# Kernel tuning notes

Hardware: AMD Instinct MI355X
Metric: run time of the kernel (lower is better)

Reference implementation:

```python
import jax, jax.numpy as jnp
import numpy as np

NEG_SLOPE = 0.2  # GATConv attention leaky_relu slope (init arg)
POST_SLOPE = 0.2  # leaky_relu after LayerNorm in outer forward
N_LAYERS = 3


def _leaky(x, slope):
    return jnp.where(x >= 0, x, slope * x)


def _layer_norm(x, g, b):
    mu = jnp.mean(x, axis=-1, keepdims=True)
    var = jnp.var(x, axis=-1, keepdims=True)
    return (x - mu) * jax.lax.rsqrt(var + 1e-5) * g + b


def _gat_conv(h, W, al, ar, bias, src, dst, apply_act):
    # DGL GATConv (eval mode, dropout = identity)
    N = h.shape[0]
    H, D = al.shape
    feat = (h @ W).reshape(N, H, D)                      # [N,H,D]
    el = jnp.einsum('nhd,hd->nh', feat, al)              # [N,H]
    er = jnp.einsum('nhd,hd->nh', feat, ar)              # [N,H]
    e = _leaky(el[src] + er[dst], NEG_SLOPE)             # [E,H] edge logits
    # segment (per-destination) softmax, numerically stable
    m = jax.ops.segment_max(e, dst, num_segments=N)      # [N,H]
    ex = jnp.exp(e - m[dst])                             # [E,H]
    s = jax.ops.segment_sum(ex, dst, num_segments=N)     # [N,H]
    alpha = ex / s[dst]                                  # [E,H]
    msg = alpha[:, :, None] * feat[src]                  # [E,H,D]
    rst = jax.ops.segment_sum(msg, dst, num_segments=N)  # [N,H,D]
    rst = rst + bias.reshape(1, H, D)
    if apply_act:
        rst = jax.nn.elu(rst)
    return rst


def setup_inputs() -> dict:
    key = jax.random.key(0)
    ks = jax.random.split(key, 12)
    N, E, IN, D, H, C = 100000, 1600000, 256, 64, 4, 40
    HID = H * D  # 256
    sc = 0.05
    return {
        'x': jax.random.normal(ks[0], (N, IN), jnp.float32),
        'W_h': jax.random.normal(ks[1], (3, IN, HID), jnp.float32) * sc,
        'attn_l_h': jax.random.normal(ks[2], (3, H, D), jnp.float32) * sc,
        'attn_r_h': jax.random.normal(ks[3], (3, H, D), jnp.float32) * sc,
        'bias_h': jnp.zeros((3, HID), jnp.float32),
        'ln_g': jnp.ones((3, HID), jnp.float32),
        'ln_b': jnp.zeros((3, HID), jnp.float32),
        'W_o': jax.random.normal(ks[4], (HID, C), jnp.float32) * sc,
        'attn_l_o': jax.random.normal(ks[5], (1, C), jnp.float32) * sc,
        'attn_r_o': jax.random.normal(ks[6], (1, C), jnp.float32) * sc,
        'bias_o': jnp.zeros((C,), jnp.float32),
        'edge_src': jax.random.randint(ks[7], (E,), 0, N, jnp.int32),
        'edge_dst': jax.random.randint(ks[8], (E,), 0, N, jnp.int32),
    }


def reference(x, W_h, attn_l_h, attn_r_h, bias_h, ln_g, ln_b,
              W_o, attn_l_o, attn_r_o, bias_o, edge_src, edge_dst):
    h = x
    for l in range(N_LAYERS):
        hn = _gat_conv(h, W_h[l], attn_l_h[l], attn_r_h[l], bias_h[l],
                       edge_src, edge_dst, True)
        hn = hn.reshape(hn.shape[0], -1)          # flatten heads -> [N, H*D]
        hn = _layer_norm(hn, ln_g[l], ln_b[l])
        hn = _leaky(hn, POST_SLOPE)
        h = hn + h if h.shape == hn.shape else hn  # residual when shapes match
    logits = _gat_conv(h, W_o, attn_l_o, attn_r_o, bias_o,
                       edge_src, edge_dst, False).sum(axis=1)  # sum over heads
    return logits
```

## Files before the change

### kernel.cpp

```cpp
#include <hip/hip_runtime.h>
#include <math.h>


#define NEG_SLOPE 0.2f

typedef __attribute__((ext_vector_type(8))) short bf16x8;
typedef __attribute__((ext_vector_type(4))) float floatx4;

__device__ __forceinline__ float leaky(float x) { return x >= 0.f ? x : NEG_SLOPE * x; }

__device__ __forceinline__ unsigned short f2bf(float f) {
    unsigned u = __builtin_bit_cast(unsigned, f);
    u += 0x7fffu + ((u >> 16) & 1u);
    return (unsigned short)(u >> 16);
}
__device__ __forceinline__ float bf2f(unsigned short h) {
    unsigned u = ((unsigned)h) << 16;
    return __builtin_bit_cast(float, u);
}

__global__ void zero_i32(int* __restrict__ p, int n) {
    int i = blockIdx.x * blockDim.x + threadIdx.x;
    if (i < n) p[i] = 0;
}

__global__ __launch_bounds__(256) void bucket_count(const int* __restrict__ dst,
                                                    int* __restrict__ bcnt, int E, int nbkt) {
    __shared__ int h[1024];
    for (int i = threadIdx.x; i < nbkt; i += 256) h[i] = 0;
    __syncthreads();
    const int base = blockIdx.x * 8192;
#pragma unroll 4
    for (int i = 0; i < 32; ++i) {
        int e = base + threadIdx.x + i * 256;
        if (e < E) atomicAdd(&h[dst[e] >> 7], 1);
    }
    __syncthreads();
    for (int i = threadIdx.x; i < nbkt; i += 256) {
        int v = h[i];
        if (v) atomicAdd(&bcnt[i], v);
    }
}

__global__ __launch_bounds__(256) void bucket_scan(const int* __restrict__ bcnt,
                                                   int* __restrict__ bbase,
                                                   int* __restrict__ bcursor, int nbkt) {
    __shared__ int s[256];
    const int t = threadIdx.x;
    int c[4];
    int tsum = 0;
#pragma unroll
    for (int j = 0; j < 4; ++j) {
        int i = t * 4 + j;
        c[j] = (i < nbkt) ? bcnt[i] : 0;
        tsum += c[j];
    }
    s[t] = tsum;
    __syncthreads();
    for (int off = 1; off < 256; off <<= 1) {
        int v = (t >= off) ? s[t - off] : 0;
        __syncthreads();
        s[t] += v;
        __syncthreads();
    }
    int excl = s[t] - tsum;
#pragma unroll
    for (int j = 0; j < 4; ++j) {
        int i = t * 4 + j;
        if (i < nbkt) {
            bbase[i] = excl;
            bcursor[i] = excl;
        }
        excl += c[j];
    }
}

__global__ __launch_bounds__(256) void bucket_partition(const int* __restrict__ src,
                                                        const int* __restrict__ dst,
                                                        int* __restrict__ bcursor,
                                                        int2* __restrict__ pairs, int E, int nbkt) {
    __shared__ int h[1024];
    __shared__ int basech[1024];
    for (int i = threadIdx.x; i < nbkt; i += 256) h[i] = 0;
    __syncthreads();
    const int base = blockIdx.x * 8192;
#pragma unroll 4
    for (int i = 0; i < 32; ++i) {
        int e = base + threadIdx.x + i * 256;
        if (e < E) atomicAdd(&h[dst[e] >> 7], 1);
    }
    __syncthreads();
    for (int i = threadIdx.x; i < nbkt; i += 256) {
        int v = h[i];
        basech[i] = v ? atomicAdd(&bcursor[i], v) : 0;
    }
    __syncthreads();
    for (int i = threadIdx.x; i < nbkt; i += 256) h[i] = 0;
    __syncthreads();
#pragma unroll 4
    for (int i = 0; i < 32; ++i) {
        int e = base + threadIdx.x + i * 256;
        if (e < E) {
            int d = dst[e], b = d >> 7;
            int r = atomicAdd(&h[b], 1);
            pairs[basech[b] + r] = make_int2(src[e], d);
        }
    }
}

__global__ __launch_bounds__(256) void csr_bucket(const int2* __restrict__ pairs,
                                                  const int* __restrict__ bbase,
                                                  int* __restrict__ start, int* __restrict__ endp,
                                                  int* __restrict__ col, int N, int E, int nbkt) {
    const int b = blockIdx.x;
    const int node0 = b << 7;
    int nc = N - node0;
    if (nc <= 0) return;
    if (nc > 128) nc = 128;
    __shared__ int cnt[128];
    __shared__ int s[128];
    const int t = threadIdx.x;
    if (t < 128) cnt[t] = 0;
    __syncthreads();
    const int ebase = bbase[b];
    const int eend = (b + 1 < nbkt) ? bbase[b + 1] : E;
    for (int e = ebase + t; e < eend; e += 256) {
        atomicAdd(&cnt[pairs[e].y - node0], 1);
    }
    __syncthreads();
    if (t < 128) s[t] = cnt[t];
    __syncthreads();
    for (int off = 1; off < 128; off <<= 1) {
        int v = 0;
        if (t < 128 && t >= off) v = s[t - off];
        __syncthreads();
        if (t < 128) s[t] += v;
        __syncthreads();
    }
    if (t < nc) {
        start[node0 + t] = ebase + s[t] - cnt[t];
        endp[node0 + t] = ebase + s[t];
    }
    if (t < 128) cnt[t] = s[t] - cnt[t];
    __syncthreads();
    for (int e = ebase + t; e < eend; e += 256) {
        int2 pr = pairs[e];
        int r = atomicAdd(&cnt[pr.y - node0], 1);
        col[ebase + r] = pr.x;
    }
}

__global__ void convert_bf(const float* __restrict__ src, unsigned short* __restrict__ dst,
                           int n4) {
    int i = blockIdx.x * blockDim.x + threadIdx.x;
    if (i < n4) {
        float4 v = *(const float4*)(src + (size_t)i * 4);
        ushort4 s;
        s.x = f2bf(v.x); s.y = f2bf(v.y); s.z = f2bf(v.z); s.w = f2bf(v.w);
        *(ushort4*)(dst + (size_t)i * 4) = s;
    }
}

__global__ void transpose_w(const float* __restrict__ W, unsigned short* __restrict__ Wt) {
    int idx = blockIdx.x * 256 + threadIdx.x;
    int l = idx >> 16, r = idx & 65535;
    int k = r >> 8, n = r & 255;
    Wt[l * 65536 + n * 256 + k] = f2bf(W[l * 65536 + k * 256 + n]);
}

__global__ void transpose_wo(const float* __restrict__ W, unsigned short* __restrict__ Wt) {
    int idx = blockIdx.x * 256 + threadIdx.x;
    int n = idx >> 8, k = idx & 255;
    Wt[n * 256 + k] = (n < 40) ? f2bf(W[k * 40 + n]) : (unsigned short)0;
}

#define BPAD 264
#define ALD 40
__global__ __launch_bounds__(512, 2) void gemm_bf16_fused(
    const unsigned short* __restrict__ A, const unsigned short* __restrict__ Wt,
    const float* __restrict__ al, const float* __restrict__ ar,
    unsigned short* __restrict__ Cb, float* __restrict__ el, float* __restrict__ er, int M) {
    __shared__ unsigned short Bs[256 * BPAD];
    __shared__ unsigned short As[2][128 * ALD];
    const int tid = threadIdx.x;
    const int lane = tid & 63, wid = tid >> 6;
    const int wm = (wid >> 2) * 64;
    const int wn = (wid & 3) * 64;
    const int q = lane >> 4, m = lane & 15;

#pragma unroll
    for (int i = 0; i < 16; ++i) {
        int flat = tid + 512 * i;
        int row = flat >> 5, col8 = (flat & 31) * 8;
        *(bf16x8*)&Bs[row * BPAD + col8] = *(const bf16x8*)(Wt + row * 256 + col8);
    }
    __syncthreads();

    const int rA = tid >> 2, k8 = (tid & 3) * 8;
    const int head = wid & 3;
    const float* alh = al + head * 64;
    const float* arh = ar + head * 64;
    const int c = lane & 15;
    float a0 = alh[c], a1 = alh[16 + c], a2 = alh[32 + c], a3 = alh[48 + c];
    float r0 = arh[c], r1 = arh[16 + c], r2 = arh[32 + c], r3 = arh[48 + c];

    const int ntiles = (M + 127) >> 7;
    for (int t = blockIdx.x; t < ntiles; t += gridDim.x) {
        const int row0 = t << 7;
        int agr = row0 + rA; if (agr >= M) agr = M - 1;
        const unsigned short* arow = A + (size_t)agr * 256 + k8;
        bf16x8 pa = *(const bf16x8*)arow;

        floatx4 acc[4][4] = {};
        int cur = 0;
        for (int kb = 0; kb < 256; kb += 32) {
            *(bf16x8*)&As[cur][rA * ALD + k8] = pa;
            __syncthreads();
            if (kb + 32 < 256) pa = *(const bf16x8*)(arow + kb + 32);
            bf16x8 af[4], bfr[4];
#pragma unroll
            for (int i = 0; i < 4; ++i) {
                af[i] = *(const bf16x8*)&As[cur][(wm + i * 16 + m) * ALD + q * 8];
                bfr[i] = *(const bf16x8*)&Bs[(wn + i * 16 + m) * BPAD + kb + q * 8];
            }
#pragma unroll
            for (int i = 0; i < 4; ++i)
#pragma unroll
                for (int j = 0; j < 4; ++j)
                    acc[i][j] = __builtin_amdgcn_mfma_f32_16x16x32_bf16(af[i], bfr[j], acc[i][j], 0, 0, 0);
            cur ^= 1;
        }

#pragma unroll
        for (int i = 0; i < 4; ++i)
#pragma unroll
            for (int j = 0; j < 4; ++j)
#pragma unroll
                for (int r = 0; r < 4; ++r) {
                    int grow = row0 + wm + i * 16 + q * 4 + r;
                    int gcol = wn + j * 16 + c;
                    if (grow < M) Cb[(size_t)grow * 256 + gcol] = f2bf(acc[i][j][r]);
                }

#pragma unroll
        for (int i = 0; i < 4; ++i)
#pragma unroll
            for (int r = 0; r < 4; ++r) {
                float pel = acc[i][0][r] * a0 + acc[i][1][r] * a1 + acc[i][2][r] * a2 + acc[i][3][r] * a3;
                float per = acc[i][0][r] * r0 + acc[i][1][r] * r1 + acc[i][2][r] * r2 + acc[i][3][r] * r3;
#pragma unroll
                for (int off = 8; off >= 1; off >>= 1) {
                    pel += __shfl_xor(pel, off);
                    per += __shfl_xor(per, off);
                }
                if (c == 0) {
                    int grow = row0 + wm + i * 16 + q * 4 + r;
                    if (grow < M) {
                        el[(size_t)grow * 4 + head] = pel;
                        er[(size_t)grow * 4 + head] = per;
                    }
                }
            }
        __syncthreads();
    }
}

#define LDSK 40
#define BSTRIDE 264
__global__ __launch_bounds__(256) void gemm_out_mfma(const unsigned short* __restrict__ h,
                                                     const unsigned short* __restrict__ Wt,
                                                     const float* __restrict__ alo,
                                                     const float* __restrict__ aro,
                                                     unsigned short* __restrict__ feat_o,
                                                     float* __restrict__ elo,
                                                     float* __restrict__ ero, int N) {
    __shared__ unsigned short As[128 * LDSK];
    __shared__ unsigned short Bs[48 * BSTRIDE];
    const int tid = threadIdx.x;
    const int row0 = blockIdx.x * 128;
    const int lane = tid & 63, wid = tid >> 6;

#pragma unroll
    for (int i = 0; i < 6; ++i) {
        int f = tid + 256 * i;
        int n = f >> 5, kk = (f & 31) * 8;
        *(bf16x8*)&Bs[n * BSTRIDE + kk] = *(const bf16x8*)(Wt + n * 256 + kk);
    }
    __syncthreads();

    floatx4 acc[2][3] = {};
    for (int kb = 0; kb < 256; kb += 32) {
#pragma unroll
        for (int i = 0; i < 2; ++i) {
            int idx = tid + 256 * i;
            int r = idx >> 2, k8 = (idx & 3) * 8;
            int gr = row0 + r;
            bf16x8 v = {};
            if (gr < N) v = *(const bf16x8*)(h + (size_t)gr * 256 + kb + k8);
            *(bf16x8*)&As[r * LDSK + k8] = v;
        }
        __syncthreads();
        const int q = lane >> 4, m = lane & 15;
        bf16x8 af[2], bfr[3];
#pragma unroll
        for (int i = 0; i < 2; ++i)
            af[i] = *(const bf16x8*)&As[(wid * 32 + i * 16 + m) * LDSK + q * 8];
#pragma unroll
        for (int j = 0; j < 3; ++j)
            bfr[j] = *(const bf16x8*)&Bs[(j * 16 + m) * BSTRIDE + kb + q * 8];
#pragma unroll
        for (int i = 0; i < 2; ++i)
#pragma unroll
            for (int j = 0; j < 3; ++j)
                acc[i][j] = __builtin_amdgcn_mfma_f32_16x16x32_bf16(af[i], bfr[j], acc[i][j], 0, 0, 0);
        __syncthreads();
    }

    const int q = lane >> 4, c = lane & 15;
#pragma unroll
    for (int i = 0; i < 2; ++i)
#pragma unroll
        for (int j = 0; j < 3; ++j)
#pragma unroll
            for (int r = 0; r < 4; ++r) {
                int grow = row0 + wid * 32 + i * 16 + q * 4 + r;
                int gcol = j * 16 + c;
                if (grow < N && gcol < 40) feat_o[(size_t)grow * 40 + gcol] = f2bf(acc[i][j][r]);
            }

    float aj[3], rj[3];
#pragma unroll
    for (int j = 0; j < 3; ++j) {
        int gcol = j * 16 + c;
        aj[j] = gcol < 40 ? alo[gcol] : 0.f;
        rj[j] = gcol < 40 ? aro[gcol] : 0.f;
    }
#pragma unroll
    for (int i = 0; i < 2; ++i)
#pragma unroll
        for (int r = 0; r < 4; ++r) {
            float pl = acc[i][0][r] * aj[0] + acc[i][1][r] * aj[1] + acc[i][2][r] * aj[2];
            float pr = acc[i][0][r] * rj[0] + acc[i][1][r] * rj[1] + acc[i][2][r] * rj[2];
#pragma unroll
            for (int off = 8; off >= 1; off >>= 1) {
                pl += __shfl_xor(pl, off);
                pr += __shfl_xor(pr, off);
            }
            if (c == 0) {
                int grow = row0 + wid * 32 + i * 16 + q * 4 + r;
                if (grow < N) {
                    elo[grow] = pl;
                    ero[grow] = pr;
                }
            }
        }
}

__global__ __launch_bounds__(256) void aggregate_hidden(
    const unsigned short* __restrict__ feat, const float* __restrict__ el,
    const float* __restrict__ er, const int* __restrict__ start, const int* __restrict__ endp,
    const int* __restrict__ col, const float* __restrict__ bias, const float* __restrict__ lng,
    const float* __restrict__ lnb, const unsigned short* __restrict__ h_in,
    unsigned short* __restrict__ h_out, int node0, int nend) {
    int node = node0 + blockIdx.x * 4 + (threadIdx.x >> 6);
    int lane = threadIdx.x & 63;
    if (node >= nend) return;
    int begin = __builtin_amdgcn_readfirstlane(start[node]);
    int end = __builtin_amdgcn_readfirstlane(endp[node]);
    const int head = lane >> 4;
    const float erh = er[(size_t)node * 4 + head];

    const int ch = lane * 4;
    const unsigned short* fbase = feat + ch;
    const size_t hstr = 256;
    float4 acc = {0.f, 0.f, 0.f, 0.f};
    float ssum = 0.f;
    int e = begin;
    for (; e + 7 < end; e += 8) {
        int sA = col[e], sB = col[e + 1], sC = col[e + 2], sD = col[e + 3];
        int sE = col[e + 4], sF = col[e + 5], sG = col[e + 6], sH = col[e + 7];
        float eA = el[(size_t)sA * 4 + head];
        float eB = el[(size_t)sB * 4 + head];
        float eC = el[(size_t)sC * 4 + head];
        float eD = el[(size_t)sD * 4 + head];
        float eE = el[(size_t)sE * 4 + head];
        float eF = el[(size_t)sF * 4 + head];
        float eG = el[(size_t)sG * 4 + head];
        float eH = el[(size_t)sH * 4 + head];
        ushort4 uA = *(const ushort4*)(fbase + sA * hstr);
        ushort4 uB = *(const ushort4*)(fbase + sB * hstr);
        ushort4 uC = *(const ushort4*)(fbase + sC * hstr);
        ushort4 uD = *(const ushort4*)(fbase + sD * hstr);
        ushort4 uE = *(const ushort4*)(fbase + sE * hstr);
        ushort4 uF = *(const ushort4*)(fbase + sF * hstr);
        ushort4 uG = *(const ushort4*)(fbase + sG * hstr);
        ushort4 uH = *(const ushort4*)(fbase + sH * hstr);
        float wA = __expf(leaky(eA + erh));
        float wB = __expf(leaky(eB + erh));
        float wC = __expf(leaky(eC + erh));
        float wD = __expf(leaky(eD + erh));
        float wE = __expf(leaky(eE + erh));
        float wF = __expf(leaky(eF + erh));
        float wG = __expf(leaky(eG + erh));
        float wH = __expf(leaky(eH + erh));
        ssum += wA + wB + wC + wD + wE + wF + wG + wH;
        acc.x = fmaf(wA, bf2f(uA.x), acc.x); acc.y = fmaf(wA, bf2f(uA.y), acc.y);
        acc.z = fmaf(wA, bf2f(uA.z), acc.z); acc.w = fmaf(wA, bf2f(uA.w), acc.w);
        acc.x = fmaf(wB, bf2f(uB.x), acc.x); acc.y = fmaf(wB, bf2f(uB.y), acc.y);
        acc.z = fmaf(wB, bf2f(uB.z), acc.z); acc.w = fmaf(wB, bf2f(uB.w), acc.w);
        acc.x = fmaf(wC, bf2f(uC.x), acc.x); acc.y = fmaf(wC, bf2f(uC.y), acc.y);
        acc.z = fmaf(wC, bf2f(uC.z), acc.z); acc.w = fmaf(wC, bf2f(uC.w), acc.w);
        acc.x = fmaf(wD, bf2f(uD.x), acc.x); acc.y = fmaf(wD, bf2f(uD.y), acc.y);
        acc.z = fmaf(wD, bf2f(uD.z), acc.z); acc.w = fmaf(wD, bf2f(uD.w), acc.w);
        acc.x = fmaf(wE, bf2f(uE.x), acc.x); acc.y = fmaf(wE, bf2f(uE.y), acc.y);
        acc.z = fmaf(wE, bf2f(uE.z), acc.z); acc.w = fmaf(wE, bf2f(uE.w), acc.w);
        acc.x = fmaf(wF, bf2f(uF.x), acc.x); acc.y = fmaf(wF, bf2f(uF.y), acc.y);
        acc.z = fmaf(wF, bf2f(uF.z), acc.z); acc.w = fmaf(wF, bf2f(uF.w), acc.w);
        acc.x = fmaf(wG, bf2f(uG.x), acc.x); acc.y = fmaf(wG, bf2f(uG.y), acc.y);
        acc.z = fmaf(wG, bf2f(uG.z), acc.z); acc.w = fmaf(wG, bf2f(uG.w), acc.w);
        acc.x = fmaf(wH, bf2f(uH.x), acc.x); acc.y = fmaf(wH, bf2f(uH.y), acc.y);
        acc.z = fmaf(wH, bf2f(uH.z), acc.z); acc.w = fmaf(wH, bf2f(uH.w), acc.w);
    }
    for (; e < end; ++e) {
        int sA = col[e];
        float wA = __expf(leaky(el[(size_t)sA * 4 + head] + erh));
        ushort4 uA = *(const ushort4*)(fbase + sA * hstr);
        ssum += wA;
        acc.x = fmaf(wA, bf2f(uA.x), acc.x); acc.y = fmaf(wA, bf2f(uA.y), acc.y);
        acc.z = fmaf(wA, bf2f(uA.z), acc.z); acc.w = fmaf(wA, bf2f(uA.w), acc.w);
    }
    float inv = ssum > 0.f ? 1.f / ssum : 0.f;
    acc.x *= inv; acc.y *= inv; acc.z *= inv; acc.w *= inv;

    float4 bb = *(const float4*)(bias + ch);
    float x0 = acc.x + bb.x, x1 = acc.y + bb.y, x2 = acc.z + bb.z, x3 = acc.w + bb.w;
    x0 = x0 > 0.f ? x0 : expm1f(x0);
    x1 = x1 > 0.f ? x1 : expm1f(x1);
    x2 = x2 > 0.f ? x2 : expm1f(x2);
    x3 = x3 > 0.f ? x3 : expm1f(x3);
    float lsum = x0 + x1 + x2 + x3;
    float lsq = x0 * x0 + x1 * x1 + x2 * x2 + x3 * x3;
#pragma unroll
    for (int off = 32; off >= 1; off >>= 1) {
        lsum += __shfl_xor(lsum, off);
        lsq += __shfl_xor(lsq, off);
    }
    float mu = lsum * (1.f / 256.f);
    float var = lsq * (1.f / 256.f) - mu * mu;
    float rstd = rsqrtf(var + 1e-5f);
    float4 g4 = *(const float4*)(lng + ch);
    float4 b4 = *(const float4*)(lnb + ch);
    ushort4 hi = *(const ushort4*)(h_in + (size_t)node * 256 + ch);
    float y0 = (x0 - mu) * rstd * g4.x + b4.x;
    float y1 = (x1 - mu) * rstd * g4.y + b4.y;
    float y2 = (x2 - mu) * rstd * g4.z + b4.z;
    float y3 = (x3 - mu) * rstd * g4.w + b4.w;
    y0 = (y0 >= 0.f ? y0 : 0.2f * y0) + bf2f(hi.x);
    y1 = (y1 >= 0.f ? y1 : 0.2f * y1) + bf2f(hi.y);
    y2 = (y2 >= 0.f ? y2 : 0.2f * y2) + bf2f(hi.z);
    y3 = (y3 >= 0.f ? y3 : 0.2f * y3) + bf2f(hi.w);
    ushort4 o;
    o.x = f2bf(y0); o.y = f2bf(y1); o.z = f2bf(y2); o.w = f2bf(y3);
    *(ushort4*)(h_out + (size_t)node * 256 + ch) = o;
}

__global__ __launch_bounds__(256) void aggregate_out(const unsigned short* __restrict__ feat_o,
                                                     const float* __restrict__ elo,
                                                     const float* __restrict__ ero,
                                                     const int* __restrict__ start,
                                                     const int* __restrict__ endp,
                                                     const int* __restrict__ col,
                                                     const float* __restrict__ bias_o,
                                                     float* __restrict__ out, int node0, int nend) {
    int node = node0 + blockIdx.x * 4 + (threadIdx.x >> 6);
    int lane = threadIdx.x & 63;
    if (node >= nend) return;
    int begin = __builtin_amdgcn_readfirstlane(start[node]);
    int end = __builtin_amdgcn_readfirstlane(endp[node]);
    float ern = ero[node];
    int cc = lane < 40 ? lane : 0;
    float acc = 0.f, ssum = 0.f;
    int e = begin;
    for (; e + 7 < end; e += 8) {
        int sA = col[e], sB = col[e + 1], sC = col[e + 2], sD = col[e + 3];
        int sE = col[e + 4], sF = col[e + 5], sG = col[e + 6], sH = col[e + 7];
        float eA = elo[sA], eB = elo[sB], eC = elo[sC], eD = elo[sD];
        float eE = elo[sE], eF = elo[sF], eG = elo[sG], eH = elo[sH];
        unsigned short fA = feat_o[(size_t)sA * 40 + cc];
        unsigned short fB = feat_o[(size_t)sB * 40 + cc];
        unsigned short fC = feat_o[(size_t)sC * 40 + cc];
        unsigned short fD = feat_o[(size_t)sD * 40 + cc];
        unsigned short fE = feat_o[(size_t)sE * 40 + cc];
        unsigned short fF = feat_o[(size_t)sF * 40 + cc];
        unsigned short fG = feat_o[(size_t)sG * 40 + cc];
        unsigned short fH = feat_o[(size_t)sH * 40 + cc];
        float wA = __expf(leaky(eA + ern));
        float wB = __expf(leaky(eB + ern));
        float wC = __expf(leaky(eC + ern));
        float wD = __expf(leaky(eD + ern));
        float wE = __expf(leaky(eE + ern));
        float wF = __expf(leaky(eF + ern));
        float wG = __expf(leaky(eG + ern));
        float wH = __expf(leaky(eH + ern));
        ssum += wA + wB + wC + wD + wE + wF + wG + wH;
        acc = fmaf(wA, bf2f(fA), acc);
        acc = fmaf(wB, bf2f(fB), acc);
        acc = fmaf(wC, bf2f(fC), acc);
        acc = fmaf(wD, bf2f(fD), acc);
        acc = fmaf(wE, bf2f(fE), acc);
        acc = fmaf(wF, bf2f(fF), acc);
        acc = fmaf(wG, bf2f(fG), acc);
        acc = fmaf(wH, bf2f(fH), acc);
    }
    for (; e < end; ++e) {
        int sA = col[e];
        float wA = __expf(leaky(elo[sA] + ern));
        ssum += wA;
        acc = fmaf(wA, bf2f(feat_o[(size_t)sA * 40 + cc]), acc);
    }
    float inv = ssum > 0.f ? 1.f / ssum : 0.f;
    if (lane < 40) out[(size_t)node * 40 + lane] = acc * inv + bias_o[lane];
}

extern "C" void kernel_launch(void* const* d_in, const int* in_sizes, int n_in,
                              void* d_out, int out_size, void* d_ws, size_t ws_size,
                              hipStream_t stream) {
    const float* x = (const float*)d_in[0];
    const float* W_h = (const float*)d_in[1];
    const float* al_h = (const float*)d_in[2];
    const float* ar_h = (const float*)d_in[3];
    const float* bias_h = (const float*)d_in[4];
    const float* ln_g = (const float*)d_in[5];
    const float* ln_b = (const float*)d_in[6];
    const float* W_o = (const float*)d_in[7];
    const float* al_o = (const float*)d_in[8];
    const float* ar_o = (const float*)d_in[9];
    const float* bias_o = (const float*)d_in[10];
    const int* esrc = (const int*)d_in[11];
    const int* edst = (const int*)d_in[12];
    const int N = in_sizes[0] / 256;
    const int E = in_sizes[11];
    float* out = (float*)d_out;

    char* ws = (char*)d_ws;
    size_t off = 0;
    auto walloc = [&](size_t bytes) -> void* {
        void* p = ws + off;
        off += (bytes + 255) & ~(size_t)255;
        return p;
    };
    unsigned short* x_bf = (unsigned short*)walloc((size_t)N * 256 * 2);
    unsigned short* h_bf = (unsigned short*)walloc((size_t)N * 256 * 2);
    unsigned short* feat_bf = (unsigned short*)walloc((size_t)N * 256 * 2);
    unsigned short* Wt = (unsigned short*)walloc((size_t)3 * 65536 * 2);
    unsigned short* Wt_o = (unsigned short*)walloc((size_t)48 * 256 * 2);
    float* el = (float*)walloc((size_t)N * 4 * 4);
    float* er = (float*)walloc((size_t)N * 4 * 4);
    int* start = (int*)walloc((size_t)N * 4);
    int* endp = (int*)walloc((size_t)N * 4);
    int* col = (int*)walloc((size_t)E * 4);
    int* bcnt = (int*)walloc(1024 * 4);
    int* bbase = (int*)walloc(1024 * 4);
    int* bcursor = (int*)walloc(1024 * 4);
    int2* pairs = (int2*)walloc((size_t)E * 8);
    if (off > ws_size) return;

    const int TB = 256;
    const int nbkt = (N + 127) >> 7;
    const int nbe = (E + 8191) / 8192;
    convert_bf<<<(N * 64 + TB - 1) / TB, TB, 0, stream>>>(x, x_bf, N * 64);
    transpose_w<<<3 * 65536 / TB, TB, 0, stream>>>(W_h, Wt);
    transpose_wo<<<48, TB, 0, stream>>>(W_o, Wt_o);
    zero_i32<<<(nbkt + TB - 1) / TB, TB, 0, stream>>>(bcnt, nbkt);
    bucket_count<<<nbe, TB, 0, stream>>>(edst, bcnt, E, nbkt);
    bucket_scan<<<1, TB, 0, stream>>>(bcnt, bbase, bcursor, nbkt);
    bucket_partition<<<nbe, TB, 0, stream>>>(esrc, edst, bcursor, pairs, E, nbkt);
    csr_bucket<<<nbkt, TB, 0, stream>>>(pairs, bbase, start, endp, col, N, E, nbkt);

    const int N2 = ((N / 2) + 3) & ~3;
    const int nbh1 = (N2 + 3) / 4;
    const int nbh2 = (N - N2 + 3) / 4;
    for (int l = 0; l < 3; ++l) {
        const unsigned short* hin = (l == 0) ? x_bf : h_bf;
        gemm_bf16_fused<<<256, 512, 0, stream>>>(hin, Wt + (size_t)l * 65536,
                                                 al_h + l * 256, ar_h + l * 256,
                                                 feat_bf, el, er, N);
        aggregate_hidden<<<nbh1, 256, 0, stream>>>(feat_bf, el, er, start, endp, col,
                                                   bias_h + l * 256, ln_g + l * 256,
                                                   ln_b + l * 256, hin, h_bf, 0, N2);
        aggregate_hidden<<<nbh2, 256, 0, stream>>>(feat_bf, el, er, start, endp, col,
                                                   bias_h + l * 256, ln_g + l * 256,
                                                   ln_b + l * 256, hin, h_bf, N2, N);
    }
    unsigned short* feat_o = feat_bf;
    float* elo = el;
    float* ero = er;
    gemm_out_mfma<<<(N + 127) / 128, 256, 0, stream>>>(h_bf, Wt_o, al_o, ar_o, feat_o, elo, ero, N);
    aggregate_out<<<nbh1, 256, 0, stream>>>(feat_o, elo, ero, start, endp, col, bias_o, out, 0, N2);
    aggregate_out<<<nbh2, 256, 0, stream>>>(feat_o, elo, ero, start, endp, col, bias_o, out, N2, N);
}
```

Baseline: 905.6 us.

## Fuse fp32-to-bf16 input conversion into first GEMM and residual read

Removes the separate convert_bf kernel: the layer-0 GEMM now reads fp32 x directly and converts to bf16 in registers, and the first aggregate reads the fp32 residual. The zero kernel is replaced by hipMemsetAsync, and the output feature stride is padded from 40 to 64 for aligned gathers. This saves one full pass over x and one launch, at the cost of doubled A-load bytes in the layer-0 GEMM and an fp32 residual read.

```diff
diff --git a/kernel.cpp b/kernel.cpp
--- a/kernel.cpp
+++ b/kernel.cpp
@@ -17,11 +17,6 @@
 __device__ __forceinline__ float bf2f(unsigned short h) {
     unsigned u = ((unsigned)h) << 16;
     return __builtin_bit_cast(float, u);
-}
-
-__global__ void zero_i32(int* __restrict__ p, int n) {
-    int i = blockIdx.x * blockDim.x + threadIdx.x;
-    if (i < n) p[i] = 0;
 }
 
 __global__ __launch_bounds__(256) void bucket_count(const int* __restrict__ dst,
@@ -150,17 +145,6 @@
     }
 }
 
-__global__ void convert_bf(const float* __restrict__ src, unsigned short* __restrict__ dst,
-                           int n4) {
-    int i = blockIdx.x * blockDim.x + threadIdx.x;
-    if (i < n4) {
-        float4 v = *(const float4*)(src + (size_t)i * 4);
-        ushort4 s;
-        s.x = f2bf(v.x); s.y = f2bf(v.y); s.z = f2bf(v.z); s.w = f2bf(v.w);
-        *(ushort4*)(dst + (size_t)i * 4) = s;
-    }
-}
-
 __global__ void transpose_w(const float* __restrict__ W, unsigned short* __restrict__ Wt) {
     int idx = blockIdx.x * 256 + threadIdx.x;
     int l = idx >> 16, r = idx & 65535;
@@ -176,10 +160,13 @@
 
 #define BPAD 264
 #define ALD 40
+template <bool F32>
 __global__ __launch_bounds__(512, 2) void gemm_bf16_fused(
-    const unsigned short* __restrict__ A, const unsigned short* __restrict__ Wt,
+    const void* __restrict__ Av, const unsigned short* __restrict__ Wt,
     const float* __restrict__ al, const float* __restrict__ ar,
     unsigned short* __restrict__ Cb, float* __restrict__ el, float* __restrict__ er, int M) {
+    const unsigned short* Ab = (const unsigned short*)Av;
+    const float* Af = (const float*)Av;
     __shared__ unsigned short Bs[256 * BPAD];
     __shared__ unsigned short As[2][128 * ALD];
     const int tid = threadIdx.x;
@@ -208,15 +195,30 @@
     for (int t = blockIdx.x; t < ntiles; t += gridDim.x) {
         const int row0 = t << 7;
         int agr = row0 + rA; if (agr >= M) agr = M - 1;
-        const unsigned short* arow = A + (size_t)agr * 256 + k8;
-        bf16x8 pa = *(const bf16x8*)arow;
-
+
+        auto loadA8 = [&](int kb) -> bf16x8 {
+            if constexpr (F32) {
+                const float* p = Af + (size_t)agr * 256 + kb + k8;
+                float4 f0 = *(const float4*)p;
+                float4 f1 = *(const float4*)(p + 4);
+                bf16x8 v;
+                v[0] = (short)f2bf(f0.x); v[1] = (short)f2bf(f0.y);
+                v[2] = (short)f2bf(f0.z); v[3] = (short)f2bf(f0.w);
+                v[4] = (short)f2bf(f1.x); v[5] = (short)f2bf(f1.y);
+                v[6] = (short)f2bf(f1.z); v[7] = (short)f2bf(f1.w);
+                return v;
+            } else {
+                return *(const bf16x8*)(Ab + (size_t)agr * 256 + kb + k8);
+            }
+        };
+
+        bf16x8 pa = loadA8(0);
         floatx4 acc[4][4] = {};
         int cur = 0;
         for (int kb = 0; kb < 256; kb += 32) {
             *(bf16x8*)&As[cur][rA * ALD + k8] = pa;
             __syncthreads();
-            if (kb + 32 < 256) pa = *(const bf16x8*)(arow + kb + 32);
+            if (kb + 32 < 256) pa = loadA8(kb + 32);
             bf16x8 af[4], bfr[4];
 #pragma unroll
             for (int i = 0; i < 4; ++i) {
@@ -267,6 +269,7 @@
 
 #define LDSK 40
 #define BSTRIDE 264
+#define OSTR 64
 __global__ __launch_bounds__(256) void gemm_out_mfma(const unsigned short* __restrict__ h,
                                                      const unsigned short* __restrict__ Wt,
                                                      const float* __restrict__ alo,
@@ -325,7 +328,7 @@
             for (int r = 0; r < 4; ++r) {
                 int grow = row0 + wid * 32 + i * 16 + q * 4 + r;
                 int gcol = j * 16 + c;
-                if (grow < N && gcol < 40) feat_o[(size_t)grow * 40 + gcol] = f2bf(acc[i][j][r]);
+                if (grow < N && gcol < 40) feat_o[(size_t)grow * OSTR + gcol] = f2bf(acc[i][j][r]);
             }
 
     float aj[3], rj[3];
@@ -361,6 +364,7 @@
     const float* __restrict__ er, const int* __restrict__ start, const int* __restrict__ endp,
     const int* __restrict__ col, const float* __restrict__ bias, const float* __restrict__ lng,
     const float* __restrict__ lnb, const unsigned short* __restrict__ h_in,
+    const float* __restrict__ h_in_f32,
     unsigned short* __restrict__ h_out, int node0, int nend) {
     int node = node0 + blockIdx.x * 4 + (threadIdx.x >> 6);
     int lane = threadIdx.x & 63;
@@ -450,15 +454,22 @@
     float rstd = rsqrtf(var + 1e-5f);
     float4 g4 = *(const float4*)(lng + ch);
     float4 b4 = *(const float4*)(lnb + ch);
-    ushort4 hi = *(const ushort4*)(h_in + (size_t)node * 256 + ch);
+    float rx, ry, rz, rw;
+    if (h_in_f32) {
+        float4 hf = *(const float4*)(h_in_f32 + (size_t)node * 256 + ch);
+        rx = hf.x; ry = hf.y; rz = hf.z; rw = hf.w;
+    } else {
+        ushort4 hi = *(const ushort4*)(h_in + (size_t)node * 256 + ch);
+        rx = bf2f(hi.x); ry = bf2f(hi.y); rz = bf2f(hi.z); rw = bf2f(hi.w);
+    }
     float y0 = (x0 - mu) * rstd * g4.x + b4.x;
     float y1 = (x1 - mu) * rstd * g4.y + b4.y;
     float y2 = (x2 - mu) * rstd * g4.z + b4.z;
     float y3 = (x3 - mu) * rstd * g4.w + b4.w;
-    y0 = (y0 >= 0.f ? y0 : 0.2f * y0) + bf2f(hi.x);
-    y1 = (y1 >= 0.f ? y1 : 0.2f * y1) + bf2f(hi.y);
-    y2 = (y2 >= 0.f ? y2 : 0.2f * y2) + bf2f(hi.z);
-    y3 = (y3 >= 0.f ? y3 : 0.2f * y3) + bf2f(hi.w);
+    y0 = (y0 >= 0.f ? y0 : 0.2f * y0) + rx;
+    y1 = (y1 >= 0.f ? y1 : 0.2f * y1) + ry;
+    y2 = (y2 >= 0.f ? y2 : 0.2f * y2) + rz;
+    y3 = (y3 >= 0.f ? y3 : 0.2f * y3) + rw;
     ushort4 o;
     o.x = f2bf(y0); o.y = f2bf(y1); o.z = f2bf(y2); o.w = f2bf(y3);
     *(ushort4*)(h_out + (size_t)node * 256 + ch) = o;
@@ -486,14 +497,14 @@
         int sE = col[e + 4], sF = col[e + 5], sG = col[e + 6], sH = col[e + 7];
         float eA = elo[sA], eB = elo[sB], eC = elo[sC], eD = elo[sD];
         float eE = elo[sE], eF = elo[sF], eG = elo[sG], eH = elo[sH];
-        unsigned short fA = feat_o[(size_t)sA * 40 + cc];
-        unsigned short fB = feat_o[(size_t)sB * 40 + cc];
-        unsigned short fC = feat_o[(size_t)sC * 40 + cc];
-        unsigned short fD = feat_o[(size_t)sD * 40 + cc];
-        unsigned short fE = feat_o[(size_t)sE * 40 + cc];
-        unsigned short fF = feat_o[(size_t)sF * 40 + cc];
-        unsigned short fG = feat_o[(size_t)sG * 40 + cc];
-        unsigned short fH = feat_o[(size_t)sH * 40 + cc];
+        unsigned short fA = feat_o[(size_t)sA * OSTR + cc];
+        unsigned short fB = feat_o[(size_t)sB * OSTR + cc];
+        unsigned short fC = feat_o[(size_t)sC * OSTR + cc];
+        unsigned short fD = feat_o[(size_t)sD * OSTR + cc];
+        unsigned short fE = feat_o[(size_t)sE * OSTR + cc];
+        unsigned short fF = feat_o[(size_t)sF * OSTR + cc];
+        unsigned short fG = feat_o[(size_t)sG * OSTR + cc];
+        unsigned short fH = feat_o[(size_t)sH * OSTR + cc];
         float wA = __expf(leaky(eA + ern));
         float wB = __expf(leaky(eB + ern));
         float wC = __expf(leaky(eC + ern));
@@ -516,7 +527,7 @@
         int sA = col[e];
         float wA = __expf(leaky(elo[sA] + ern));
         ssum += wA;
-        acc = fmaf(wA, bf2f(feat_o[(size_t)sA * 40 + cc]), acc);
+        acc = fmaf(wA, bf2f(feat_o[(size_t)sA * OSTR + cc]), acc);
     }
     float inv = ssum > 0.f ? 1.f / ssum : 0.f;
     if (lane < 40) out[(size_t)node * 40 + lane] = acc * inv + bias_o[lane];
@@ -549,7 +560,6 @@
         off += (bytes + 255) & ~(size_t)255;
         return p;
     };
-    unsigned short* x_bf = (unsigned short*)walloc((size_t)N * 256 * 2);
     unsigned short* h_bf = (unsigned short*)walloc((size_t)N * 256 * 2);
     unsigned short* feat_bf = (unsigned short*)walloc((size_t)N * 256 * 2);
     unsigned short* Wt = (unsigned short*)walloc((size_t)3 * 65536 * 2);
@@ -568,10 +578,9 @@
     const int TB = 256;
     const int nbkt = (N + 127) >> 7;
     const int nbe = (E + 8191) / 8192;
-    convert_bf<<<(N * 64 + TB - 1) / TB, TB, 0, stream>>>(x, x_bf, N * 64);
     transpose_w<<<3 * 65536 / TB, TB, 0, stream>>>(W_h, Wt);
     transpose_wo<<<48, TB, 0, stream>>>(W_o, Wt_o);
-    zero_i32<<<(nbkt + TB - 1) / TB, TB, 0, stream>>>(bcnt, nbkt);
+    hipMemsetAsync(bcnt, 0, (size_t)nbkt * 4, stream);
     bucket_count<<<nbe, TB, 0, stream>>>(edst, bcnt, E, nbkt);
     bucket_scan<<<1, TB, 0, stream>>>(bcnt, bbase, bcursor, nbkt);
     bucket_partition<<<nbe, TB, 0, stream>>>(esrc, edst, bcursor, pairs, E, nbkt);
@@ -581,16 +590,23 @@
     const int nbh1 = (N2 + 3) / 4;
     const int nbh2 = (N - N2 + 3) / 4;
     for (int l = 0; l < 3; ++l) {
-        const unsigned short* hin = (l == 0) ? x_bf : h_bf;
-        gemm_bf16_fused<<<256, 512, 0, stream>>>(hin, Wt + (size_t)l * 65536,
-                                                 al_h + l * 256, ar_h + l * 256,
-                                                 feat_bf, el, er, N);
+        if (l == 0) {
+            gemm_bf16_fused<true><<<256, 512, 0, stream>>>(x, Wt,
+                                                           al_h, ar_h,
+                                                           feat_bf, el, er, N);
+        } else {
+            gemm_bf16_fused<false><<<256, 512, 0, stream>>>(h_bf, Wt + (size_t)l * 65536,
+                                                            al_h + l * 256, ar_h + l * 256,
+                                                            feat_bf, el, er, N);
+        }
+        const unsigned short* hin_bf = h_bf;
+        const float* hin_f32 = (l == 0) ? x : nullptr;
         aggregate_hidden<<<nbh1, 256, 0, stream>>>(feat_bf, el, er, start, endp, col,
                                                    bias_h + l * 256, ln_g + l * 256,
-                                                   ln_b + l * 256, hin, h_bf, 0, N2);
+                                                   ln_b + l * 256, hin_bf, hin_f32, h_bf, 0, N2);
         aggregate_hidden<<<nbh2, 256, 0, stream>>>(feat_bf, el, er, start, endp, col,
                                                    bias_h + l * 256, ln_g + l * 256,
-                                                   ln_b + l * 256, hin, h_bf, N2, N);
+                                                   ln_b + l * 256, hin_bf, hin_f32, h_bf, N2, N);
     }
     unsigned short* feat_o = feat_bf;
     float* elo = el;
```

Measured after the change: 908.6 us. About the same (+0.3%).
